# Kernel tuning notes

Hardware: AMD Instinct MI355X
Metric: run time of the kernel (lower is better)

Reference implementation:

```python
import jax, jax.numpy as jnp
import numpy as np

N, M, D_K, D_V = 8192, 8192, 128, 128
SCALING = 1.0 / D_K  # module uses 1/d_k, NOT 1/sqrt(d_k)


def setup_inputs() -> dict:
    key = jax.random.key(0)
    kq, kk, kv = jax.random.split(key, 3)
    Q = jax.random.normal(kq, (N, D_K), dtype=jnp.float32)
    K = jax.random.normal(kk, (M, D_K), dtype=jnp.float32)
    V = jax.random.normal(kv, (M, D_V), dtype=jnp.float32)
    return {"Q": Q, "K": K, "V": V}


def reference(Q, K, V):
    # dots = Q @ K^T * (1/d_k)  -> [N, M]
    dots = jnp.einsum("nd,md->nm", Q, K) * SCALING
    # softmax over keys; dropout p=0 is identity
    attn = jax.nn.softmax(dots, axis=-1)
    # output = attn @ V -> [N, d_v]
    return jnp.einsum("nm,mv->nv", attn, V)
```

## Files before the change

### kernel.cpp

```cpp
#include <hip/hip_runtime.h>
#include <hip/hip_bf16.h>
#include <cstdint>
#include <cstddef>


typedef __attribute__((ext_vector_type(8))) short short8;
typedef __attribute__((ext_vector_type(4))) short shortx4;
typedef __attribute__((ext_vector_type(4))) float floatx4;
typedef __attribute__((ext_vector_type(16))) float floatx16;
typedef __attribute__((ext_vector_type(8))) _Float16 half8;

#define N_Q    8192
#define N_KV   8192
#define DHEAD  128
#define BK     64
#define QSCALE (1.4426950408889634f / 128.0f)

static __device__ __forceinline__ unsigned short f2bf(float x) {
  __hip_bfloat16 h = __float2bfloat16(x);
  unsigned short u;
  __builtin_memcpy(&u, &h, 2);
  return u;
}

static __device__ __forceinline__ uint32_t trunc_pack(float a, float b) {
  uint32_t ua, ub;
  __builtin_memcpy(&ua, &a, 4);
  __builtin_memcpy(&ub, &b, 4);
  return (ua >> 16) | (ub & 0xffff0000u);
}

#define MFMA32(a, b, c) __builtin_amdgcn_mfma_f32_32x32x16_bf16((a), (b), (c), 0, 0, 0)

#define GLD_LDS16(g, l)                                                        \
  __builtin_amdgcn_global_load_lds(                                            \
      (const __attribute__((address_space(1))) void*)(g),                      \
      (__attribute__((address_space(3))) void*)(l), 16, 0, 0)

__global__ void cvt_kernel(const float* __restrict__ K,
                           const float* __restrict__ V,
                           unsigned short* __restrict__ Kbc,
                           unsigned short* __restrict__ Vtc) {
  int bid = blockIdx.x;
  if (bid < 512) {
    int tid = bid * 256 + threadIdx.x;
    int ki = tid & 63;
    int ch = (tid >> 6) & 15;
    int b  = tid >> 10;
    const float* src = K + ((size_t)(b * 64 + ki) * DHEAD + ch * 8);
    floatx4 f0 = *(const floatx4*)src;
    floatx4 f1 = *(const floatx4*)(src + 4);
    short8 o;
    o[0] = (short)f2bf(f0[0]); o[1] = (short)f2bf(f0[1]);
    o[2] = (short)f2bf(f0[2]); o[3] = (short)f2bf(f0[3]);
    o[4] = (short)f2bf(f1[0]); o[5] = (short)f2bf(f1[1]);
    o[6] = (short)f2bf(f1[2]); o[7] = (short)f2bf(f1[3]);
    *(short8*)(Kbc + (size_t)tid * 8) = o;
  } else {
    int tid = (bid - 512) * 256 + threadIdx.x;
    int kh = tid & 1;
    int dv = (tid >> 1) & 127;
    int c2 = (tid >> 8) & 7;
    int b  = tid >> 11;
    int k0 = b * 64 + c2 * 8 + kh * 4;
    shortx4 o;
    o[0] = (short)f2bf(V[(size_t)(k0 + 0) * DHEAD + dv]);
    o[1] = (short)f2bf(V[(size_t)(k0 + 1) * DHEAD + dv]);
    o[2] = (short)f2bf(V[(size_t)(k0 + 2) * DHEAD + dv]);
    o[3] = (short)f2bf(V[(size_t)(k0 + 3) * DHEAD + dv]);
    *(shortx4*)(Vtc + (size_t)tid * 4) = o;
  }
}

__global__ __launch_bounds__(256, 3) void attn_kernel(
    const float* __restrict__ Q, const unsigned short* __restrict__ Kbc,
    const unsigned short* __restrict__ Vtc, _Float16* __restrict__ Opart,
    float* __restrict__ Lst) {
  __shared__ unsigned short Ks[8192];
  __shared__ unsigned short Vts[8192];

  const int t = threadIdx.x;
  const int w = t >> 6;
  const int lane = t & 63;
  const int h = lane >> 5;
  const int c = lane & 31;
  const int qbase = blockIdx.x * 128 + w * 32;
  const int sp = blockIdx.y;
  const int nsp = gridDim.y;
  const int NT = (N_KV / BK) / nsp;
  const int kb0 = sp * NT;

  short8 qf[8];
  {
    const float* qrow = Q + (size_t)(qbase + c) * DHEAD + h * 8;
#pragma unroll
    for (int dc = 0; dc < 8; ++dc) {
      floatx4 f0 = *(const floatx4*)(qrow + dc * 16);
      floatx4 f1 = *(const floatx4*)(qrow + dc * 16 + 4);
      short8 s;
      s[0] = (short)f2bf(f0[0] * QSCALE); s[1] = (short)f2bf(f0[1] * QSCALE);
      s[2] = (short)f2bf(f0[2] * QSCALE); s[3] = (short)f2bf(f0[3] * QSCALE);
      s[4] = (short)f2bf(f1[0] * QSCALE); s[5] = (short)f2bf(f1[1] * QSCALE);
      s[6] = (short)f2bf(f1[2] * QSCALE); s[7] = (short)f2bf(f1[3] * QSCALE);
      qf[dc] = s;
    }
  }

  floatx16 acc[4];
#pragma unroll
  for (int i = 0; i < 4; ++i)
#pragma unroll
    for (int r = 0; r < 16; ++r) acc[i][r] = 0.f;
  float lsum = 0.f;

  const unsigned short* kp = Kbc + (size_t)kb0 * 8192 + (w * 4) * 512 + lane * 8;
  const unsigned short* vp = Vtc + (size_t)kb0 * 8192 + (w * 4) * 512 + lane * 8;
  unsigned short* kdst = Ks + (w * 4) * 512;
  unsigned short* vdst = Vts + (w * 4) * 512;

  for (int it = 0; it < NT; ++it) {
#pragma unroll
    for (int i = 0; i < 4; ++i) {
      GLD_LDS16(kp + i * 512, kdst + i * 512);
      GLD_LDS16(vp + i * 512, vdst + i * 512);
    }
    kp += 8192;
    vp += 8192;
    __syncthreads();

    const short8* KsF = (const short8*)Ks;
    const short8* VtsF = (const short8*)Vts;

#pragma unroll
    for (int st = 0; st < 2; ++st) {
      floatx16 sc;
#pragma unroll
      for (int r = 0; r < 16; ++r) sc[r] = 0.f;
#pragma unroll
      for (int dc = 0; dc < 8; ++dc) {
        short8 a = KsF[(dc * 2 + h) * 64 + st * 32 + c];
        sc = MFMA32(a, qf[dc], sc);
      }
      uint32_t qd[8];
#pragma unroll
      for (int r2 = 0; r2 < 4; ++r2) {
        float p0 = exp2f(sc[r2 * 4 + 0]);
        float p1 = exp2f(sc[r2 * 4 + 1]);
        float p2 = exp2f(sc[r2 * 4 + 2]);
        float p3 = exp2f(sc[r2 * 4 + 3]);
        lsum += (p0 + p1) + (p2 + p3);
        qd[r2 * 2 + 0] = trunc_pack(p0, p1);
        qd[r2 * 2 + 1] = trunc_pack(p2, p3);
      }
#pragma unroll
      for (int b = 0; b < 2; ++b) {
        uint32_t s0 = h ? qd[(2 * b) * 2 + 0] : qd[(2 * b + 1) * 2 + 0];
        uint32_t s1 = h ? qd[(2 * b) * 2 + 1] : qd[(2 * b + 1) * 2 + 1];
        uint32_t r0 = __shfl_xor(s0, 32, 64);
        uint32_t r1 = __shfl_xor(s1, 32, 64);
        uint32_t o0 = h ? qd[(2 * b + 1) * 2 + 0] : qd[(2 * b) * 2 + 0];
        uint32_t o1 = h ? qd[(2 * b + 1) * 2 + 1] : qd[(2 * b) * 2 + 1];
        uint32_t f[4];
        f[0] = h ? r0 : o0;
        f[1] = h ? r1 : o1;
        f[2] = h ? o0 : r0;
        f[3] = h ? o1 : r1;
        short8 pf;
        __builtin_memcpy(&pf, f, 16);
        const int kc = st * 2 + b;
#pragma unroll
        for (int nb = 0; nb < 4; ++nb) {
          short8 bv = VtsF[(kc * 2 + h) * 128 + nb * 32 + c];
          acc[nb] = MFMA32(pf, bv, acc[nb]);
        }
      }
    }
    __syncthreads();
  }

  lsum += __shfl_xor(lsum, 32, 64);
  if (h == 0) Lst[(size_t)sp * N_Q + qbase + c] = lsum;
  _Float16* op = Opart + ((size_t)sp * N_Q + qbase) * DHEAD;
#pragma unroll
  for (int nb = 0; nb < 4; ++nb)
#pragma unroll
    for (int r = 0; r < 16; ++r) {
      int row = (r & 3) + 8 * (r >> 2) + 4 * h;
      op[(size_t)row * DHEAD + nb * 32 + c] = (_Float16)acc[nb][r];
    }
}

__global__ void merge_kernel(const _Float16* __restrict__ Opart,
                             const float* __restrict__ Lst,
                             float* __restrict__ out, int nsp) {
  int tid = blockIdx.x * blockDim.x + threadIdx.x;
  int g = tid >> 4;
  int d0 = (tid & 15) * 8;
  float den = 0.f;
  float num[8] = {0.f, 0.f, 0.f, 0.f, 0.f, 0.f, 0.f, 0.f};
  for (int s = 0; s < nsp; ++s) {
    den += Lst[(size_t)s * N_Q + g];
    half8 o = *(const half8*)(Opart + ((size_t)s * N_Q + g) * DHEAD + d0);
#pragma unroll
    for (int j = 0; j < 8; ++j) num[j] += (float)o[j];
  }
  float inv = 1.0f / den;
  floatx4 r0 = (floatx4){num[0] * inv, num[1] * inv, num[2] * inv, num[3] * inv};
  floatx4 r1 = (floatx4){num[4] * inv, num[5] * inv, num[6] * inv, num[7] * inv};
  float* dst = out + (size_t)g * DHEAD + d0;
  *(floatx4*)dst = r0;
  *(floatx4*)(dst + 4) = r1;
}

extern "C" void kernel_launch(void* const* d_in, const int* in_sizes, int n_in,
                              void* d_out, int out_size, void* d_ws,
                              size_t ws_size, hipStream_t stream) {
  const float* Q = (const float*)d_in[0];
  const float* K = (const float*)d_in[1];
  const float* V = (const float*)d_in[2];
  float* out = (float*)d_out;

  const size_t need16 = (4ull << 20) + 16ull * N_Q * DHEAD * 2 + 16ull * N_Q * 4;
  const int nsp = (ws_size >= need16) ? 16 : 8;

  char* ws = (char*)d_ws;
  unsigned short* Kbc = (unsigned short*)(ws);
  unsigned short* Vtc = (unsigned short*)(ws + (2u << 20));
  _Float16* Opart = (_Float16*)(ws + (4u << 20));
  float* Lst = (float*)(ws + (4ull << 20) + (size_t)nsp * N_Q * DHEAD * 2);

  cvt_kernel<<<dim3(1536), dim3(256), 0, stream>>>(K, V, Kbc, Vtc);
  attn_kernel<<<dim3(N_Q / 128, nsp), dim3(256), 0, stream>>>(Q, Kbc, Vtc,
                                                              Opart, Lst);
  merge_kernel<<<dim3(512), dim3(256), 0, stream>>>(Opart, Lst, out, nsp);
}
```

Measured before the change: 121.7 us.

## Process two 32-row query sub-tiles per wave to reuse K/V fragments

Each wave now handles 64 query rows as two 32-row sub-tiles, so every K and V fragment read from LDS feeds two MFMAs instead of one. The block covers 256 queries and the grid halves in x, which halves the total K/V global-to-LDS traffic. The cost is doubled accumulator and Q registers, so launch bounds drop to two blocks per CU and occupancy falls. The grid also shrinks to 32x16 blocks, which may underfill the CUs.

```diff
diff --git a/kernel.cpp b/kernel.cpp
--- a/kernel.cpp
+++ b/kernel.cpp
@@ -72,7 +72,7 @@
   }
 }
 
-__global__ __launch_bounds__(256, 3) void attn_kernel(
+__global__ __launch_bounds__(256, 2) void attn_kernel(
     const float* __restrict__ Q, const unsigned short* __restrict__ Kbc,
     const unsigned short* __restrict__ Vtc, _Float16* __restrict__ Opart,
     float* __restrict__ Lst) {
@@ -84,15 +84,16 @@
   const int lane = t & 63;
   const int h = lane >> 5;
   const int c = lane & 31;
-  const int qbase = blockIdx.x * 128 + w * 32;
+  const int qbase = blockIdx.x * 256 + w * 64;
   const int sp = blockIdx.y;
   const int nsp = gridDim.y;
   const int NT = (N_KV / BK) / nsp;
   const int kb0 = sp * NT;
 
-  short8 qf[8];
-  {
-    const float* qrow = Q + (size_t)(qbase + c) * DHEAD + h * 8;
+  short8 qf[2][8];
+#pragma unroll
+  for (int qs = 0; qs < 2; ++qs) {
+    const float* qrow = Q + (size_t)(qbase + qs * 32 + c) * DHEAD + h * 8;
 #pragma unroll
     for (int dc = 0; dc < 8; ++dc) {
       floatx4 f0 = *(const floatx4*)(qrow + dc * 16);
@@ -102,16 +103,18 @@
       s[2] = (short)f2bf(f0[2] * QSCALE); s[3] = (short)f2bf(f0[3] * QSCALE);
       s[4] = (short)f2bf(f1[0] * QSCALE); s[5] = (short)f2bf(f1[1] * QSCALE);
       s[6] = (short)f2bf(f1[2] * QSCALE); s[7] = (short)f2bf(f1[3] * QSCALE);
-      qf[dc] = s;
+      qf[qs][dc] = s;
     }
   }
 
-  floatx16 acc[4];
-#pragma unroll
-  for (int i = 0; i < 4; ++i)
-#pragma unroll
-    for (int r = 0; r < 16; ++r) acc[i][r] = 0.f;
-  float lsum = 0.f;
+  floatx16 acc[2][4];
+#pragma unroll
+  for (int qs = 0; qs < 2; ++qs)
+#pragma unroll
+    for (int i = 0; i < 4; ++i)
+#pragma unroll
+      for (int r = 0; r < 16; ++r) acc[qs][i][r] = 0.f;
+  float lsum[2] = {0.f, 0.f};
 
   const unsigned short* kp = Kbc + (size_t)kb0 * 8192 + (w * 4) * 512 + lane * 8;
   const unsigned short* vp = Vtc + (size_t)kb0 * 8192 + (w * 4) * 512 + lane * 8;
@@ -133,61 +136,73 @@
 
 #pragma unroll
     for (int st = 0; st < 2; ++st) {
-      floatx16 sc;
-#pragma unroll
-      for (int r = 0; r < 16; ++r) sc[r] = 0.f;
-#pragma unroll
-      for (int dc = 0; dc < 8; ++dc) {
-        short8 a = KsF[(dc * 2 + h) * 64 + st * 32 + c];
-        sc = MFMA32(a, qf[dc], sc);
+      uint32_t qd[2][8];
+#pragma unroll
+      for (int qs = 0; qs < 2; ++qs) {
+        floatx16 sc;
+#pragma unroll
+        for (int r = 0; r < 16; ++r) sc[r] = 0.f;
+#pragma unroll
+        for (int dc = 0; dc < 8; ++dc) {
+          short8 a = KsF[(dc * 2 + h) * 64 + st * 32 + c];
+          sc = MFMA32(a, qf[qs][dc], sc);
+        }
+#pragma unroll
+        for (int r2 = 0; r2 < 4; ++r2) {
+          float p0 = exp2f(sc[r2 * 4 + 0]);
+          float p1 = exp2f(sc[r2 * 4 + 1]);
+          float p2 = exp2f(sc[r2 * 4 + 2]);
+          float p3 = exp2f(sc[r2 * 4 + 3]);
+          lsum[qs] += (p0 + p1) + (p2 + p3);
+          qd[qs][r2 * 2 + 0] = trunc_pack(p0, p1);
+          qd[qs][r2 * 2 + 1] = trunc_pack(p2, p3);
+        }
       }
-      uint32_t qd[8];
-#pragma unroll
-      for (int r2 = 0; r2 < 4; ++r2) {
-        float p0 = exp2f(sc[r2 * 4 + 0]);
-        float p1 = exp2f(sc[r2 * 4 + 1]);
-        float p2 = exp2f(sc[r2 * 4 + 2]);
-        float p3 = exp2f(sc[r2 * 4 + 3]);
-        lsum += (p0 + p1) + (p2 + p3);
-        qd[r2 * 2 + 0] = trunc_pack(p0, p1);
-        qd[r2 * 2 + 1] = trunc_pack(p2, p3);
-      }
 #pragma unroll
       for (int b = 0; b < 2; ++b) {
-        uint32_t s0 = h ? qd[(2 * b) * 2 + 0] : qd[(2 * b + 1) * 2 + 0];
-        uint32_t s1 = h ? qd[(2 * b) * 2 + 1] : qd[(2 * b + 1) * 2 + 1];
-        uint32_t r0 = __shfl_xor(s0, 32, 64);
-        uint32_t r1 = __shfl_xor(s1, 32, 64);
-        uint32_t o0 = h ? qd[(2 * b + 1) * 2 + 0] : qd[(2 * b) * 2 + 0];
-        uint32_t o1 = h ? qd[(2 * b + 1) * 2 + 1] : qd[(2 * b) * 2 + 1];
-        uint32_t f[4];
-        f[0] = h ? r0 : o0;
-        f[1] = h ? r1 : o1;
-        f[2] = h ? o0 : r0;
-        f[3] = h ? o1 : r1;
-        short8 pf;
-        __builtin_memcpy(&pf, f, 16);
+        short8 pf[2];
+#pragma unroll
+        for (int qs = 0; qs < 2; ++qs) {
+          uint32_t s0 = h ? qd[qs][(2 * b) * 2 + 0] : qd[qs][(2 * b + 1) * 2 + 0];
+          uint32_t s1 = h ? qd[qs][(2 * b) * 2 + 1] : qd[qs][(2 * b + 1) * 2 + 1];
+          uint32_t r0 = __shfl_xor(s0, 32, 64);
+          uint32_t r1 = __shfl_xor(s1, 32, 64);
+          uint32_t o0 = h ? qd[qs][(2 * b + 1) * 2 + 0] : qd[qs][(2 * b) * 2 + 0];
+          uint32_t o1 = h ? qd[qs][(2 * b + 1) * 2 + 1] : qd[qs][(2 * b) * 2 + 1];
+          uint32_t f[4];
+          f[0] = h ? r0 : o0;
+          f[1] = h ? r1 : o1;
+          f[2] = h ? o0 : r0;
+          f[3] = h ? o1 : r1;
+          __builtin_memcpy(&pf[qs], f, 16);
+        }
         const int kc = st * 2 + b;
 #pragma unroll
         for (int nb = 0; nb < 4; ++nb) {
           short8 bv = VtsF[(kc * 2 + h) * 128 + nb * 32 + c];
-          acc[nb] = MFMA32(pf, bv, acc[nb]);
+          acc[0][nb] = MFMA32(pf[0], bv, acc[0][nb]);
+          acc[1][nb] = MFMA32(pf[1], bv, acc[1][nb]);
         }
       }
     }
     __syncthreads();
   }
 
-  lsum += __shfl_xor(lsum, 32, 64);
-  if (h == 0) Lst[(size_t)sp * N_Q + qbase + c] = lsum;
+#pragma unroll
+  for (int qs = 0; qs < 2; ++qs) {
+    float l = lsum[qs] + __shfl_xor(lsum[qs], 32, 64);
+    if (h == 0) Lst[(size_t)sp * N_Q + qbase + qs * 32 + c] = l;
+  }
   _Float16* op = Opart + ((size_t)sp * N_Q + qbase) * DHEAD;
 #pragma unroll
-  for (int nb = 0; nb < 4; ++nb)
-#pragma unroll
-    for (int r = 0; r < 16; ++r) {
-      int row = (r & 3) + 8 * (r >> 2) + 4 * h;
-      op[(size_t)row * DHEAD + nb * 32 + c] = (_Float16)acc[nb][r];
-    }
+  for (int qs = 0; qs < 2; ++qs)
+#pragma unroll
+    for (int nb = 0; nb < 4; ++nb)
+#pragma unroll
+      for (int r = 0; r < 16; ++r) {
+        int row = qs * 32 + (r & 3) + 8 * (r >> 2) + 4 * h;
+        op[(size_t)row * DHEAD + nb * 32 + c] = (_Float16)acc[qs][nb][r];
+      }
 }
 
 __global__ void merge_kernel(const _Float16* __restrict__ Opart,
@@ -230,7 +245,7 @@
   float* Lst = (float*)(ws + (4ull << 20) + (size_t)nsp * N_Q * DHEAD * 2);
 
   cvt_kernel<<<dim3(1536), dim3(256), 0, stream>>>(K, V, Kbc, Vtc);
-  attn_kernel<<<dim3(N_Q / 128, nsp), dim3(256), 0, stream>>>(Q, Kbc, Vtc,
+  attn_kernel<<<dim3(N_Q / 256, nsp), dim3(256), 0, stream>>>(Q, Kbc, Vtc,
                                                               Opart, Lst);
   merge_kernel<<<dim3(512), dim3(256), 0, stream>>>(Opart, Lst, out, nsp);
 }
```

After: 142.7 us. +17.3%, slower.

## Fuse convert, attention and merge into one persistent kernel with grid barriers

Applied to the files above, without the earlier changes.

Replaces the three launches (K/V bf16 conversion, split-KV attention, merge) with a single 512-block kernel that uses atomic grid-wide barriers between phases. The split count is fixed at 8 instead of choosing 16 when workspace allows, and V transposition now writes 8 elements per thread. This is meant to remove launch gaps and tail idle time between kernels. The cost is spin-wait barriers that need all 512 blocks co-resident, which the launch bounds of 2 blocks per CU are set to allow, plus a memset launch for the counter and less parallelism in the attention phase.

```diff
diff --git a/kernel.cpp b/kernel.cpp
--- a/kernel.cpp
+++ b/kernel.cpp
@@ -5,7 +5,6 @@
 
 
 typedef __attribute__((ext_vector_type(8))) short short8;
-typedef __attribute__((ext_vector_type(4))) short shortx4;
 typedef __attribute__((ext_vector_type(4))) float floatx4;
 typedef __attribute__((ext_vector_type(16))) float floatx16;
 typedef __attribute__((ext_vector_type(8))) _Float16 half8;
@@ -13,7 +12,9 @@
 #define N_Q    8192
 #define N_KV   8192
 #define DHEAD  128
+#define NSPLIT 8
 #define BK     64
+#define GRID_BLOCKS 512
 #define QSCALE (1.4426950408889634f / 128.0f)
 
 static __device__ __forceinline__ unsigned short f2bf(float x) {
@@ -37,13 +38,34 @@
       (const __attribute__((address_space(1))) void*)(g),                      \
       (__attribute__((address_space(3))) void*)(l), 16, 0, 0)
 
-__global__ void cvt_kernel(const float* __restrict__ K,
-                           const float* __restrict__ V,
-                           unsigned short* __restrict__ Kbc,
-                           unsigned short* __restrict__ Vtc) {
-  int bid = blockIdx.x;
-  if (bid < 512) {
-    int tid = bid * 256 + threadIdx.x;
+static __device__ __forceinline__ void grid_barrier(unsigned int* cnt) {
+  __syncthreads();
+  if (threadIdx.x == 0) {
+    __threadfence();
+    __hip_atomic_fetch_add(cnt, 1u, __ATOMIC_RELEASE, __HIP_MEMORY_SCOPE_AGENT);
+    int guard = 0;
+    while (__hip_atomic_load(cnt, __ATOMIC_ACQUIRE, __HIP_MEMORY_SCOPE_AGENT) <
+           GRID_BLOCKS) {
+      __builtin_amdgcn_s_sleep(8);
+      if (++guard > (1 << 20)) break;
+    }
+    __threadfence();
+  }
+  __syncthreads();
+}
+
+__global__ __launch_bounds__(256, 2) void fused_kernel(
+    const float* __restrict__ Q, const float* __restrict__ K,
+    const float* __restrict__ V, unsigned short* __restrict__ Kbc,
+    unsigned short* __restrict__ Vtc, _Float16* __restrict__ Opart,
+    float* __restrict__ Lst, float* __restrict__ out,
+    unsigned int* __restrict__ bar) {
+  __shared__ unsigned short Ks[8192];
+  __shared__ unsigned short Vts[8192];
+
+  const int tid = blockIdx.x * 256 + threadIdx.x;
+
+  {
     int ki = tid & 63;
     int ch = (tid >> 6) & 15;
     int b  = tid >> 10;
@@ -56,160 +78,156 @@
     o[4] = (short)f2bf(f1[0]); o[5] = (short)f2bf(f1[1]);
     o[6] = (short)f2bf(f1[2]); o[7] = (short)f2bf(f1[3]);
     *(short8*)(Kbc + (size_t)tid * 8) = o;
-  } else {
-    int tid = (bid - 512) * 256 + threadIdx.x;
-    int kh = tid & 1;
-    int dv = (tid >> 1) & 127;
-    int c2 = (tid >> 8) & 7;
-    int b  = tid >> 11;
-    int k0 = b * 64 + c2 * 8 + kh * 4;
-    shortx4 o;
-    o[0] = (short)f2bf(V[(size_t)(k0 + 0) * DHEAD + dv]);
-    o[1] = (short)f2bf(V[(size_t)(k0 + 1) * DHEAD + dv]);
-    o[2] = (short)f2bf(V[(size_t)(k0 + 2) * DHEAD + dv]);
-    o[3] = (short)f2bf(V[(size_t)(k0 + 3) * DHEAD + dv]);
-    *(shortx4*)(Vtc + (size_t)tid * 4) = o;
-  }
-}
-
-__global__ __launch_bounds__(256, 3) void attn_kernel(
-    const float* __restrict__ Q, const unsigned short* __restrict__ Kbc,
-    const unsigned short* __restrict__ Vtc, _Float16* __restrict__ Opart,
-    float* __restrict__ Lst) {
-  __shared__ unsigned short Ks[8192];
-  __shared__ unsigned short Vts[8192];
-
-  const int t = threadIdx.x;
-  const int w = t >> 6;
-  const int lane = t & 63;
-  const int h = lane >> 5;
-  const int c = lane & 31;
-  const int qbase = blockIdx.x * 128 + w * 32;
-  const int sp = blockIdx.y;
-  const int nsp = gridDim.y;
-  const int NT = (N_KV / BK) / nsp;
-  const int kb0 = sp * NT;
-
-  short8 qf[8];
+
+    int dv = tid & 127;
+    int c2 = (tid >> 7) & 7;
+    int vb = tid >> 10;
+    int k0 = vb * 64 + c2 * 8;
+    const float* vsrc = V + (size_t)k0 * DHEAD + dv;
+    short8 vo;
+#pragma unroll
+    for (int kk = 0; kk < 8; ++kk)
+      vo[kk] = (short)f2bf(vsrc[(size_t)kk * DHEAD]);
+    *(short8*)(Vtc + (size_t)tid * 8) = vo;
+  }
+  grid_barrier(bar + 16);
+
   {
-    const float* qrow = Q + (size_t)(qbase + c) * DHEAD + h * 8;
-#pragma unroll
-    for (int dc = 0; dc < 8; ++dc) {
-      floatx4 f0 = *(const floatx4*)(qrow + dc * 16);
-      floatx4 f1 = *(const floatx4*)(qrow + dc * 16 + 4);
-      short8 s;
-      s[0] = (short)f2bf(f0[0] * QSCALE); s[1] = (short)f2bf(f0[1] * QSCALE);
-      s[2] = (short)f2bf(f0[2] * QSCALE); s[3] = (short)f2bf(f0[3] * QSCALE);
-      s[4] = (short)f2bf(f1[0] * QSCALE); s[5] = (short)f2bf(f1[1] * QSCALE);
-      s[6] = (short)f2bf(f1[2] * QSCALE); s[7] = (short)f2bf(f1[3] * QSCALE);
-      qf[dc] = s;
-    }
-  }
-
-  floatx16 acc[4];
-#pragma unroll
-  for (int i = 0; i < 4; ++i)
-#pragma unroll
-    for (int r = 0; r < 16; ++r) acc[i][r] = 0.f;
-  float lsum = 0.f;
-
-  const unsigned short* kp = Kbc + (size_t)kb0 * 8192 + (w * 4) * 512 + lane * 8;
-  const unsigned short* vp = Vtc + (size_t)kb0 * 8192 + (w * 4) * 512 + lane * 8;
-  unsigned short* kdst = Ks + (w * 4) * 512;
-  unsigned short* vdst = Vts + (w * 4) * 512;
-
-  for (int it = 0; it < NT; ++it) {
-#pragma unroll
-    for (int i = 0; i < 4; ++i) {
-      GLD_LDS16(kp + i * 512, kdst + i * 512);
-      GLD_LDS16(vp + i * 512, vdst + i * 512);
-    }
-    kp += 8192;
-    vp += 8192;
-    __syncthreads();
-
-    const short8* KsF = (const short8*)Ks;
-    const short8* VtsF = (const short8*)Vts;
-
-#pragma unroll
-    for (int st = 0; st < 2; ++st) {
-      floatx16 sc;
-#pragma unroll
-      for (int r = 0; r < 16; ++r) sc[r] = 0.f;
+    const int t = threadIdx.x;
+    const int w = t >> 6;
+    const int lane = t & 63;
+    const int h = lane >> 5;
+    const int c = lane & 31;
+    const int qx = blockIdx.x & 63;
+    const int sp = blockIdx.x >> 6;
+    const int qbase = qx * 128 + w * 32;
+    const int NT = (N_KV / BK) / NSPLIT;
+    const int kb0 = sp * NT;
+
+    short8 qf[8];
+    {
+      const float* qrow = Q + (size_t)(qbase + c) * DHEAD + h * 8;
 #pragma unroll
       for (int dc = 0; dc < 8; ++dc) {
-        short8 a = KsF[(dc * 2 + h) * 64 + st * 32 + c];
-        sc = MFMA32(a, qf[dc], sc);
-      }
-      uint32_t qd[8];
-#pragma unroll
-      for (int r2 = 0; r2 < 4; ++r2) {
-        float p0 = exp2f(sc[r2 * 4 + 0]);
-        float p1 = exp2f(sc[r2 * 4 + 1]);
-        float p2 = exp2f(sc[r2 * 4 + 2]);
-        float p3 = exp2f(sc[r2 * 4 + 3]);
-        lsum += (p0 + p1) + (p2 + p3);
-        qd[r2 * 2 + 0] = trunc_pack(p0, p1);
-        qd[r2 * 2 + 1] = trunc_pack(p2, p3);
-      }
-#pragma unroll
-      for (int b = 0; b < 2; ++b) {
-        uint32_t s0 = h ? qd[(2 * b) * 2 + 0] : qd[(2 * b + 1) * 2 + 0];
-        uint32_t s1 = h ? qd[(2 * b) * 2 + 1] : qd[(2 * b + 1) * 2 + 1];
-        uint32_t r0 = __shfl_xor(s0, 32, 64);
-        uint32_t r1 = __shfl_xor(s1, 32, 64);
-        uint32_t o0 = h ? qd[(2 * b + 1) * 2 + 0] : qd[(2 * b) * 2 + 0];
-        uint32_t o1 = h ? qd[(2 * b + 1) * 2 + 1] : qd[(2 * b) * 2 + 1];
-        uint32_t f[4];
-        f[0] = h ? r0 : o0;
-        f[1] = h ? r1 : o1;
-        f[2] = h ? o0 : r0;
-        f[3] = h ? o1 : r1;
-        short8 pf;
-        __builtin_memcpy(&pf, f, 16);
-        const int kc = st * 2 + b;
-#pragma unroll
-        for (int nb = 0; nb < 4; ++nb) {
-          short8 bv = VtsF[(kc * 2 + h) * 128 + nb * 32 + c];
-          acc[nb] = MFMA32(pf, bv, acc[nb]);
+        floatx4 f0 = *(const floatx4*)(qrow + dc * 16);
+        floatx4 f1 = *(const floatx4*)(qrow + dc * 16 + 4);
+        short8 s;
+        s[0] = (short)f2bf(f0[0] * QSCALE); s[1] = (short)f2bf(f0[1] * QSCALE);
+        s[2] = (short)f2bf(f0[2] * QSCALE); s[3] = (short)f2bf(f0[3] * QSCALE);
+        s[4] = (short)f2bf(f1[0] * QSCALE); s[5] = (short)f2bf(f1[1] * QSCALE);
+        s[6] = (short)f2bf(f1[2] * QSCALE); s[7] = (short)f2bf(f1[3] * QSCALE);
+        qf[dc] = s;
+      }
+    }
+
+    floatx16 acc[4];
+#pragma unroll
+    for (int i = 0; i < 4; ++i)
+#pragma unroll
+      for (int r = 0; r < 16; ++r) acc[i][r] = 0.f;
+    float lsum = 0.f;
+
+    const unsigned short* kp =
+        Kbc + (size_t)kb0 * 8192 + (w * 4) * 512 + lane * 8;
+    const unsigned short* vp =
+        Vtc + (size_t)kb0 * 8192 + (w * 4) * 512 + lane * 8;
+    unsigned short* kdst = Ks + (w * 4) * 512;
+    unsigned short* vdst = Vts + (w * 4) * 512;
+
+    for (int it = 0; it < NT; ++it) {
+#pragma unroll
+      for (int i = 0; i < 4; ++i) {
+        GLD_LDS16(kp + i * 512, kdst + i * 512);
+        GLD_LDS16(vp + i * 512, vdst + i * 512);
+      }
+      kp += 8192;
+      vp += 8192;
+      __syncthreads();
+
+      const short8* KsF = (const short8*)Ks;
+      const short8* VtsF = (const short8*)Vts;
+
+#pragma unroll
+      for (int st = 0; st < 2; ++st) {
+        floatx16 sc;
+#pragma unroll
+        for (int r = 0; r < 16; ++r) sc[r] = 0.f;
+#pragma unroll
+        for (int dc = 0; dc < 8; ++dc) {
+          short8 a = KsF[(dc * 2 + h) * 64 + st * 32 + c];
+          sc = MFMA32(a, qf[dc], sc);
         }
-      }
-    }
-    __syncthreads();
-  }
-
-  lsum += __shfl_xor(lsum, 32, 64);
-  if (h == 0) Lst[(size_t)sp * N_Q + qbase + c] = lsum;
-  _Float16* op = Opart + ((size_t)sp * N_Q + qbase) * DHEAD;
-#pragma unroll
-  for (int nb = 0; nb < 4; ++nb)
-#pragma unroll
-    for (int r = 0; r < 16; ++r) {
-      int row = (r & 3) + 8 * (r >> 2) + 4 * h;
-      op[(size_t)row * DHEAD + nb * 32 + c] = (_Float16)acc[nb][r];
-    }
-}
-
-__global__ void merge_kernel(const _Float16* __restrict__ Opart,
-                             const float* __restrict__ Lst,
-                             float* __restrict__ out, int nsp) {
-  int tid = blockIdx.x * blockDim.x + threadIdx.x;
-  int g = tid >> 4;
-  int d0 = (tid & 15) * 8;
-  float den = 0.f;
-  float num[8] = {0.f, 0.f, 0.f, 0.f, 0.f, 0.f, 0.f, 0.f};
-  for (int s = 0; s < nsp; ++s) {
-    den += Lst[(size_t)s * N_Q + g];
-    half8 o = *(const half8*)(Opart + ((size_t)s * N_Q + g) * DHEAD + d0);
-#pragma unroll
-    for (int j = 0; j < 8; ++j) num[j] += (float)o[j];
-  }
-  float inv = 1.0f / den;
-  floatx4 r0 = (floatx4){num[0] * inv, num[1] * inv, num[2] * inv, num[3] * inv};
-  floatx4 r1 = (floatx4){num[4] * inv, num[5] * inv, num[6] * inv, num[7] * inv};
-  float* dst = out + (size_t)g * DHEAD + d0;
-  *(floatx4*)dst = r0;
-  *(floatx4*)(dst + 4) = r1;
+        uint32_t qd[8];
+#pragma unroll
+        for (int r2 = 0; r2 < 4; ++r2) {
+          float p0 = exp2f(sc[r2 * 4 + 0]);
+          float p1 = exp2f(sc[r2 * 4 + 1]);
+          float p2 = exp2f(sc[r2 * 4 + 2]);
+          float p3 = exp2f(sc[r2 * 4 + 3]);
+          lsum += (p0 + p1) + (p2 + p3);
+          qd[r2 * 2 + 0] = trunc_pack(p0, p1);
+          qd[r2 * 2 + 1] = trunc_pack(p2, p3);
+        }
+#pragma unroll
+        for (int b = 0; b < 2; ++b) {
+          uint32_t s0 = h ? qd[(2 * b) * 2 + 0] : qd[(2 * b + 1) * 2 + 0];
+          uint32_t s1 = h ? qd[(2 * b) * 2 + 1] : qd[(2 * b + 1) * 2 + 1];
+          uint32_t r0 = __shfl_xor(s0, 32, 64);
+          uint32_t r1 = __shfl_xor(s1, 32, 64);
+          uint32_t o0 = h ? qd[(2 * b + 1) * 2 + 0] : qd[(2 * b) * 2 + 0];
+          uint32_t o1 = h ? qd[(2 * b + 1) * 2 + 1] : qd[(2 * b) * 2 + 1];
+          uint32_t f[4];
+          f[0] = h ? r0 : o0;
+          f[1] = h ? r1 : o1;
+          f[2] = h ? o0 : r0;
+          f[3] = h ? o1 : r1;
+          short8 pf;
+          __builtin_memcpy(&pf, f, 16);
+          const int kc = st * 2 + b;
+#pragma unroll
+          for (int nb = 0; nb < 4; ++nb) {
+            short8 bv = VtsF[(kc * 2 + h) * 128 + nb * 32 + c];
+            acc[nb] = MFMA32(pf, bv, acc[nb]);
+          }
+        }
+      }
+      __syncthreads();
+    }
+
+    lsum += __shfl_xor(lsum, 32, 64);
+    if (h == 0) Lst[(size_t)sp * N_Q + qbase + c] = lsum;
+    _Float16* op = Opart + ((size_t)sp * N_Q + qbase) * DHEAD;
+#pragma unroll
+    for (int nb = 0; nb < 4; ++nb)
+#pragma unroll
+      for (int r = 0; r < 16; ++r) {
+        int row = (r & 3) + 8 * (r >> 2) + 4 * h;
+        op[(size_t)row * DHEAD + nb * 32 + c] = (_Float16)acc[nb][r];
+      }
+  }
+  grid_barrier(bar + 32);
+
+  {
+    int g = tid >> 4;
+    int d0 = (tid & 15) * 8;
+    float den = 0.f;
+    float num[8] = {0.f, 0.f, 0.f, 0.f, 0.f, 0.f, 0.f, 0.f};
+#pragma unroll
+    for (int s = 0; s < NSPLIT; ++s) {
+      den += Lst[(size_t)s * N_Q + g];
+      half8 o = *(const half8*)(Opart + ((size_t)s * N_Q + g) * DHEAD + d0);
+#pragma unroll
+      for (int j = 0; j < 8; ++j) num[j] += (float)o[j];
+    }
+    float inv = 1.0f / den;
+    floatx4 r0 =
+        (floatx4){num[0] * inv, num[1] * inv, num[2] * inv, num[3] * inv};
+    floatx4 r1 =
+        (floatx4){num[4] * inv, num[5] * inv, num[6] * inv, num[7] * inv};
+    float* dst = out + (size_t)g * DHEAD + d0;
+    *(floatx4*)dst = r0;
+    *(floatx4*)(dst + 4) = r1;
+  }
 }
 
 extern "C" void kernel_launch(void* const* d_in, const int* in_sizes, int n_in,
@@ -220,17 +238,14 @@
   const float* V = (const float*)d_in[2];
   float* out = (float*)d_out;
 
-  const size_t need16 = (4ull << 20) + 16ull * N_Q * DHEAD * 2 + 16ull * N_Q * 4;
-  const int nsp = (ws_size >= need16) ? 16 : 8;
-
   char* ws = (char*)d_ws;
   unsigned short* Kbc = (unsigned short*)(ws);
   unsigned short* Vtc = (unsigned short*)(ws + (2u << 20));
   _Float16* Opart = (_Float16*)(ws + (4u << 20));
-  float* Lst = (float*)(ws + (4ull << 20) + (size_t)nsp * N_Q * DHEAD * 2);
-
-  cvt_kernel<<<dim3(1536), dim3(256), 0, stream>>>(K, V, Kbc, Vtc);
-  attn_kernel<<<dim3(N_Q / 128, nsp), dim3(256), 0, stream>>>(Q, Kbc, Vtc,
-                                                              Opart, Lst);
-  merge_kernel<<<dim3(512), dim3(256), 0, stream>>>(Opart, Lst, out, nsp);
-}
+  float* Lst = (float*)(ws + (20u << 20));
+  unsigned int* bar = (unsigned int*)(ws + (20u << 20) + (1u << 18));
+
+  hipMemsetAsync(bar, 0, 256, stream);
+  fused_kernel<<<dim3(GRID_BLOCKS), dim3(256), 0, stream>>>(
+      Q, K, V, Kbc, Vtc, Opart, Lst, out, bar);
+}
```

New measurement: 262.4 us. 116% more time.
